# Kernel tuning notes

Measured on AMD Instinct MI355X. Metric: run time of the kernel, lower is better.

Reference implementation:

```python
import jax, jax.numpy as jnp
import numpy as np

B = 4096
IN_DIMS = (3, 32, 32)      # in_numel = 3072
OUT_DIMS = (64, 16, 16)    # out_numel = 16384
IN_NUMEL = int(np.prod(IN_DIMS))
OUT_NUMEL = int(np.prod(OUT_DIMS))


def setup_inputs() -> dict:
    key = jax.random.key(0)
    k1, k2, k3, k4 = jax.random.split(key, 4)
    x = jax.random.normal(k1, (B,) + IN_DIMS, dtype=jnp.float32)
    # Cached composed linear operator (out_numel x in_numel); scale ~1/sqrt(fan_in)
    cached_matrix = jax.random.normal(k2, (OUT_NUMEL, IN_NUMEL), dtype=jnp.float32) / np.sqrt(IN_NUMEL)
    cached_matrix_extra = jax.random.uniform(k3, (1,), dtype=jnp.float32) + 0.5
    cached_tensor_extra = jax.random.normal(k4, (IN_NUMEL, IN_NUMEL), dtype=jnp.float32) / IN_NUMEL
    return {
        "x": x,
        "cached_matrix": cached_matrix,
        "cached_matrix_extra": cached_matrix_extra,
        "cached_tensor_extra": cached_tensor_extra,
    }


def reference(x, cached_matrix, cached_matrix_extra, cached_tensor_extra):
    batches = x.shape[0]
    # input_as_matrix: [in_numel, B]
    X = x.reshape(batches, -1).T
    # input_as_matrix_extra: L2 norm per column -> [1, B]
    X_extra = jnp.linalg.norm(X, ord=2, axis=0, keepdims=True)
    # output_as_matrix = M @ X : [out_numel, B]
    Y = jnp.matmul(cached_matrix, X)
    # output_as_matrix_extra = s * ||x|| + sum((T @ X) * X, axis=0)
    Y_extra = cached_matrix_extra * X_extra + jnp.sum(jnp.matmul(cached_tensor_extra, X) * X, axis=0, keepdims=True)
    Y = Y / Y_extra
    return Y.T.reshape(batches, *OUT_DIMS)
```

## Files before the change

kernel.cpp:

```cpp
#include <hip/hip_runtime.h>
#include <hip/hip_bf16.h>

typedef __attribute__((ext_vector_type(8))) short bf16x8;
typedef __attribute__((ext_vector_type(4))) short bf16x4;
typedef __attribute__((ext_vector_type(4))) float f32x4;

#define DEV __device__ __forceinline__

static constexpr int BATCH = 4096;
static constexpr int KDIM  = 3072;
static constexpr int NOUT  = 16384;

DEV unsigned short f2bf(float f) {
  union { float f; unsigned int u; } v; v.f = f;
  unsigned int u = v.u;
  u += 0x7fffu + ((u >> 16) & 1u);
  return (unsigned short)(u >> 16);
}

DEV float bf2f(unsigned short h) {
  union { unsigned int u; float f; } v;
  v.u = ((unsigned int)h) << 16;
  return v.f;
}

__global__ __launch_bounds__(256) void prep_x_kernel(
    const float* __restrict__ x, unsigned short* __restrict__ xbf,
    float* __restrict__ nrm) {
  const int b = blockIdx.x;
  const int t = threadIdx.x;
  const float* row = x + (size_t)b * KDIM;
  unsigned short* orow = xbf + (size_t)b * KDIM;
  float ss = 0.f;
#pragma unroll
  for (int i = 0; i < 3; ++i) {
    const int c = i * 256 + t;
    float4 v = reinterpret_cast<const float4*>(row)[c];
    ss += v.x * v.x + v.y * v.y + v.z * v.z + v.w * v.w;
    bf16x4 o;
    o[0] = (short)f2bf(v.x); o[1] = (short)f2bf(v.y);
    o[2] = (short)f2bf(v.z); o[3] = (short)f2bf(v.w);
    reinterpret_cast<bf16x4*>(orow)[c] = o;
  }
#pragma unroll
  for (int off = 32; off > 0; off >>= 1) ss += __shfl_down(ss, off, 64);
  __shared__ float red[4];
  if ((t & 63) == 0) red[t >> 6] = ss;
  __syncthreads();
  if (t == 0) nrm[b] = sqrtf(red[0] + red[1] + red[2] + red[3]);
}

__global__ __launch_bounds__(256) void cvt_kernel(
    const float* __restrict__ src, unsigned short* __restrict__ dst, size_t n4) {
  size_t i = (size_t)blockIdx.x * blockDim.x + threadIdx.x;
  const size_t stride = (size_t)gridDim.x * blockDim.x;
  for (; i < n4; i += stride) {
    float4 v = reinterpret_cast<const float4*>(src)[i];
    bf16x4 o;
    o[0] = (short)f2bf(v.x); o[1] = (short)f2bf(v.y);
    o[2] = (short)f2bf(v.z); o[3] = (short)f2bf(v.w);
    reinterpret_cast<bf16x4*>(dst)[i] = o;
  }
}

__global__ __launch_bounds__(256) void finalize_ye_kernel(
    const float* __restrict__ nrm, const float* __restrict__ partial,
    const float* __restrict__ sp, float* __restrict__ ye) {
  const int b = blockIdx.x * blockDim.x + threadIdx.x;
  if (b >= BATCH) return;
  float qv = 0.f;
#pragma unroll
  for (int i = 0; i < 48; ++i) qv += partial[(size_t)b * 48 + i];
  ye[b] = sp[0] * nrm[b] + qv;
}

static constexpr int BK8 = 64;

#define LDSE(BUF, OP, HALF) ((BUF)*32768 + (OP)*16384 + (HALF)*8192)

#define STAGE8(OP, HALF, S, BUF)                                             \
  {                                                                          \
    const unsigned short* gb_ = (OP) ? Bm : A;                               \
    const int gr0_ = ((OP) ? col0 : row0) + (HALF)*128;                      \
    _Pragma("unroll")                                                        \
    for (int j_ = 0; j_ < 2; ++j_) {                                         \
      const int row_ = j_*64 + wid*8 + (lane >> 3);                          \
      const int le_  = ((lane & 7)*8) ^ ((row_ & 7) << 3);                   \
      __builtin_amdgcn_global_load_lds(                                      \
        (const __attribute__((address_space(1))) unsigned int*)(const void*) \
          (gb_ + (size_t)(gr0_ + row_)*KDIM + (S)*BK8 + le_),                \
        (__attribute__((address_space(3))) unsigned int*)(void*)             \
          (lds + LDSE(BUF, OP, HALF) + j_*4096 + wid*512),                   \
        16, 0, 0);                                                           \
    }                                                                        \
  }

#define LOADA8(P, QM, DST)                                                   \
  _Pragma("unroll")                                                          \
  for (int mi = 0; mi < 4; ++mi) {                                           \
    const int r_ = wm*64 + mi*16 + (lane & 15);                              \
    const int xv_ = (r_ & 7) << 3;                                           \
    _Pragma("unroll")                                                        \
    for (int ks = 0; ks < 2; ++ks)                                           \
      DST[mi][ks] = *reinterpret_cast<const bf16x8*>(                        \
          lds + LDSE(P, 0, QM) + ((r_*64 + ks*32 + (lane >> 4)*8) ^ xv_));   \
  }

#define LOADB8(P, QN, DST)                                                   \
  _Pragma("unroll")                                                          \
  for (int ni = 0; ni < 2; ++ni) {                                           \
    const int r_ = wn*32 + ni*16 + (lane & 15);                              \
    const int xv_ = (r_ & 7) << 3;                                           \
    _Pragma("unroll")                                                        \
    for (int ks = 0; ks < 2; ++ks)                                           \
      DST[ni][ks] = *reinterpret_cast<const bf16x8*>(                        \
          lds + LDSE(P, 1, QN) + ((r_*64 + ks*32 + (lane >> 4)*8) ^ xv_));   \
  }

#define MMA8(QM, QN, ASRC, BSRC)                                             \
  __builtin_amdgcn_s_setprio(1);                                             \
  _Pragma("unroll")                                                          \
  for (int mi = 0; mi < 4; ++mi)                                             \
    _Pragma("unroll")                                                        \
    for (int ni = 0; ni < 2; ++ni)                                           \
      _Pragma("unroll")                                                      \
      for (int ks = 0; ks < 2; ++ks)                                         \
        acc[(QM)*4 + mi][(QN)*2 + ni] =                                      \
            __builtin_amdgcn_mfma_f32_16x16x32_bf16(                         \
                ASRC[mi][ks], BSRC[ni][ks], acc[(QM)*4 + mi][(QN)*2 + ni],   \
                0, 0, 0);                                                    \
  __builtin_amdgcn_s_setprio(0);

#define VMW(N)                                                               \
  asm volatile("s_waitcnt vmcnt(" #N ")" ::: "memory");                      \
  __builtin_amdgcn_sched_barrier(0)

#define BARR __builtin_amdgcn_s_barrier()

#define TILE9(P, T)                                                          \
  LOADA8(P, 0, aft); LOADB8(P, 0, bft0);                                     \
  STAGE8(1, 1, (T)+1, (P)^1);                                                \
  BARR;                                                                      \
  STAGE8(1, 0, (T)+1, (P)^1);                                                \
  MMA8(0, 0, aft, bft0);                                                     \
  LOADB8(P, 1, bft1);                                                        \
  BARR;                                                                      \
  STAGE8(0, 0, (T)+2, P);                                                    \
  MMA8(0, 1, aft, bft1);                                                     \
  LOADA8(P, 1, aft);                                                         \
  BARR;                                                                      \
  MMA8(1, 1, aft, bft1);                                                     \
  BARR;                                                                      \
  STAGE8(0, 1, (T)+2, P);                                                    \
  MMA8(1, 0, aft, bft0);                                                     \
  VMW(4);                                                                    \
  BARR;

#define LGKMW8 asm volatile("s_waitcnt lgkmcnt(8)" ::: "memory")

#define TILE8Q(P, T)                                                         \
  LOADA8(P, 0, aft); LOADB8(P, 0, bft0);                                     \
  STAGE8(1, 1, (T)+1, (P)^1);                                                \
  LGKMW8;                                                                    \
  BARR; MMA8(0, 0, aft, bft0); BARR;                                         \
  LOADB8(P, 1, bft1);                                                        \
  STAGE8(1, 0, (T)+1, (P)^1);                                                \
  BARR; MMA8(0, 1, aft, bft1); BARR;                                         \
  LOADA8(P, 1, aft);                                                         \
  STAGE8(0, 0, (T)+2, P);                                                    \
  BARR; MMA8(1, 1, aft, bft1); BARR;                                         \
  STAGE8(0, 1, (T)+2, P);                                                    \
  BARR; MMA8(1, 0, aft, bft0); VMW(4); BARR;

#define PROLOG8Q(T0)                                                         \
  STAGE8(0, 0, (T0), 0); STAGE8(1, 0, (T0), 0);                              \
  STAGE8(0, 1, (T0), 0); STAGE8(1, 1, (T0), 0);                              \
  STAGE8(0, 0, (T0)+1, 1); STAGE8(0, 1, (T0)+1, 1);                          \
  VMW(4);                                                                    \
  BARR;

#define TAIL8Q(TE)                                                           \
  LOADA8(0, 0, aft); LOADB8(0, 0, bft0);                                     \
  STAGE8(1, 1, (TE)+1, 1);                                                   \
  BARR; MMA8(0, 0, aft, bft0); BARR;                                         \
  LOADB8(0, 1, bft1);                                                        \
  STAGE8(1, 0, (TE)+1, 1);                                                   \
  BARR; MMA8(0, 1, aft, bft1); BARR;                                         \
  LOADA8(0, 1, aft);                                                         \
  BARR; MMA8(1, 1, aft, bft1); BARR;                                         \
  MMA8(1, 0, aft, bft0); VMW(0); BARR;                                       \
  LOADA8(1, 0, aft); LOADB8(1, 0, bft0);                                     \
  BARR; MMA8(0, 0, aft, bft0); BARR;                                         \
  LOADB8(1, 1, bft1);                                                        \
  BARR; MMA8(0, 1, aft, bft1); BARR;                                         \
  LOADA8(1, 1, aft);                                                         \
  BARR; MMA8(1, 1, aft, bft1); BARR;                                         \
  MMA8(1, 0, aft, bft0);

__global__ __launch_bounds__(512) void gemm8_kernel(
    const unsigned short* __restrict__ A,
    const unsigned short* __restrict__ Bm,
    const float* __restrict__ ye,
    float* __restrict__ out) {
  __shared__ unsigned short lds[65536];
  const int t = threadIdx.x;
  const int lane = t & 63, wid = t >> 6;
  const int wm = wid >> 2, wn = wid & 3;

  const int bid = blockIdx.x;
  const int xcd = bid & 7, r = bid >> 3;
  const int by = r >> 3;
  const int bx = xcd * 8 + (r & 7);
  const int row0 = by * 256, col0 = bx * 256;

  f32x4 acc[8][4];
#pragma unroll
  for (int i = 0; i < 8; ++i)
#pragma unroll
    for (int j = 0; j < 4; ++j) acc[i][j] = (f32x4){0.f, 0.f, 0.f, 0.f};

  bf16x8 aft[4][2], bft0[2][2], bft1[2][2];

  STAGE8(1, 1, 0, 0); STAGE8(1, 0, 0, 0);
  STAGE8(0, 0, 0, 0); STAGE8(0, 1, 0, 0);
  STAGE8(0, 0, 1, 1); STAGE8(0, 1, 1, 1);
  VMW(4);
  BARR;

#pragma unroll 1
  for (int i = 0; i < 23; ++i) {
    const int t0 = 2 * i;
    TILE9(0, t0);
    TILE9(1, t0 + 1);
  }

  LOADA8(0, 0, aft); LOADB8(0, 0, bft0);
  STAGE8(1, 1, 47, 1);
  BARR;
  STAGE8(1, 0, 47, 1);
  MMA8(0, 0, aft, bft0);
  LOADB8(0, 1, bft1);
  BARR;
  MMA8(0, 1, aft, bft1);
  LOADA8(0, 1, aft);
  BARR;
  MMA8(1, 1, aft, bft1);
  BARR;
  MMA8(1, 0, aft, bft0);
  VMW(0);
  BARR;
  LOADA8(1, 0, aft); LOADB8(1, 0, bft0);
  BARR;
  MMA8(0, 0, aft, bft0);
  LOADB8(1, 1, bft1);
  BARR;
  MMA8(0, 1, aft, bft1);
  LOADA8(1, 1, aft);
  BARR;
  MMA8(1, 1, aft, bft1);
  BARR;
  MMA8(1, 0, aft, bft0);

#pragma unroll
  for (int am = 0; am < 8; ++am) {
#pragma unroll
    for (int j = 0; j < 4; ++j) {
      const int b = row0 + (am >> 2) * 128 + wm * 64 + (am & 3) * 16 +
                    (lane >> 4) * 4 + j;
      const float rr = 1.0f / ye[b];
      float* orow = out + (size_t)b * NOUT + col0;
#pragma unroll
      for (int an = 0; an < 4; ++an)
        orow[(an >> 1) * 128 + wn * 32 + (an & 1) * 16 + (lane & 15)] =
            acc[am][an][j] * rr;
    }
  }
}

__global__ __launch_bounds__(512) void qform8_kernel(
    const unsigned short* __restrict__ A,
    const unsigned short* __restrict__ Bm,
    float* __restrict__ partial) {
  __shared__ unsigned short lds[65536];
  const int t = threadIdx.x;
  const int lane = t & 63, wid = t >> 6;
  const int wm = wid >> 2, wn = wid & 3;

  const int bid = blockIdx.x;
  const int wgid = (bid & 7) * 96 + (bid >> 3);
  const int jt = wgid / 64;
  const int rem = wgid % 64;
  const int bt = rem >> 2;
  const int ks4 = rem & 3;
  const int row0 = bt * 256, col0 = jt * 256;
  const int k0t = ks4 * 12;

  f32x4 acc[8][4];
#pragma unroll
  for (int i = 0; i < 8; ++i)
#pragma unroll
    for (int j = 0; j < 4; ++j) acc[i][j] = (f32x4){0.f, 0.f, 0.f, 0.f};

  bf16x8 aft[4][2], bft0[2][2], bft1[2][2];

  PROLOG8Q(k0t);
#pragma unroll 1
  for (int i = 0; i < 5; ++i) {
    const int t0 = k0t + 2 * i;
    TILE8Q(0, t0);
    TILE8Q(1, t0 + 1);
  }
  TAIL8Q(k0t + 10);

  float* sred = reinterpret_cast<float*>(lds);
#pragma unroll
  for (int am = 0; am < 8; ++am) {
#pragma unroll
    for (int j = 0; j < 4; ++j) {
      const int b = row0 + (am >> 2) * 128 + wm * 64 + (am & 3) * 16 +
                    (lane >> 4) * 4 + j;
      float s = 0.f;
#pragma unroll
      for (int an = 0; an < 4; ++an) {
        const int col = col0 + (an >> 1) * 128 + wn * 32 + (an & 1) * 16 +
                        (lane & 15);
        s += acc[am][an][j] * bf2f(A[(size_t)b * KDIM + col]);
      }
      s += __shfl_xor(s, 1, 64);
      s += __shfl_xor(s, 2, 64);
      s += __shfl_xor(s, 4, 64);
      s += __shfl_xor(s, 8, 64);
      if ((lane & 15) == 0)
        sred[wid * 128 + am * 16 + j * 4 + (lane >> 4)] = s;
    }
  }
  __syncthreads();
  if (t < 256) {
    const int wmI = t >> 7, idx = t & 127;
    const int am = idx >> 4, j = (idx >> 2) & 3, lp = idx & 3;
    const int b = row0 + (am >> 2) * 128 + wmI * 64 + (am & 3) * 16 + lp * 4 + j;
    float s = 0.f;
#pragma unroll
    for (int w2 = 0; w2 < 4; ++w2) s += sred[(wmI * 4 + w2) * 128 + idx];
    partial[(size_t)b * 48 + jt * 4 + ks4] = s;
  }
}

__global__ __launch_bounds__(256) void main_gemm_kernel(
    const unsigned short* __restrict__ A,
    const float* __restrict__ Bf,
    const float* __restrict__ ye,
    float* __restrict__ out) {
  __shared__ unsigned short ldsA[128 * 32];
  __shared__ unsigned short ldsB[128 * 32];
  const int t = threadIdx.x;
  const int lane = t & 63;
  const int wv = t >> 6;
  const int wr = wv >> 1, wc = wv & 1;
  const int col0 = blockIdx.x * 128;
  const int row0 = blockIdx.y * 128;

  f32x4 acc[4][4];
#pragma unroll
  for (int i = 0; i < 4; ++i)
#pragma unroll
    for (int j = 0; j < 4; ++j) acc[i][j] = (f32x4){0.f, 0.f, 0.f, 0.f};

  const unsigned short* aBase = A + (size_t)row0 * KDIM;
  const float* bfBase = Bf + (size_t)col0 * KDIM;
  const int ldsoff0 = (t & ~63) * 8;

  for (int k0 = 0; k0 < KDIM; k0 += 32) {
    __syncthreads();
#pragma unroll
    for (int i = 0; i < 2; ++i) {
      const int c = i * 256 + t;
      const unsigned short* ga = aBase + (size_t)(c >> 2) * KDIM + (k0 + (c & 3) * 8);
      __builtin_amdgcn_global_load_lds(
          (const __attribute__((address_space(1))) unsigned int*)(const void*)ga,
          (__attribute__((address_space(3))) unsigned int*)(void*)(ldsA + i * 2048 + ldsoff0),
          16, 0, 0);
    }
#pragma unroll
    for (int i = 0; i < 2; ++i) {
      const int c = i * 256 + t;
      const int r = c >> 1, ko = (c & 1) * 16;
      const float* gp = bfBase + (size_t)r * KDIM + k0 + ko;
      unsigned short tmp[16];
#pragma unroll
      for (int q = 0; q < 4; ++q) {
        float4 v = reinterpret_cast<const float4*>(gp)[q];
        tmp[q * 4 + 0] = f2bf(v.x); tmp[q * 4 + 1] = f2bf(v.y);
        tmp[q * 4 + 2] = f2bf(v.z); tmp[q * 4 + 3] = f2bf(v.w);
      }
#pragma unroll
      for (int q = 0; q < 2; ++q)
        *reinterpret_cast<bf16x8*>(&ldsB[r * 32 + ko + q * 8]) =
            *reinterpret_cast<const bf16x8*>(&tmp[q * 8]);
    }
    __syncthreads();
    bf16x8 af[4], bfr[4];
#pragma unroll
    for (int mi = 0; mi < 4; ++mi)
      af[mi] = *reinterpret_cast<const bf16x8*>(
          &ldsA[(wr * 64 + mi * 16 + (lane & 15)) * 32 + (lane >> 4) * 8]);
#pragma unroll
    for (int ni = 0; ni < 4; ++ni)
      bfr[ni] = *reinterpret_cast<const bf16x8*>(
          &ldsB[(wc * 64 + ni * 16 + (lane & 15)) * 32 + (lane >> 4) * 8]);
#pragma unroll
    for (int mi = 0; mi < 4; ++mi)
#pragma unroll
      for (int ni = 0; ni < 4; ++ni)
        acc[mi][ni] = __builtin_amdgcn_mfma_f32_16x16x32_bf16(af[mi], bfr[ni], acc[mi][ni], 0, 0, 0);
  }

#pragma unroll
  for (int mi = 0; mi < 4; ++mi) {
#pragma unroll
    for (int j = 0; j < 4; ++j) {
      const int b = row0 + wr * 64 + mi * 16 + (lane >> 4) * 4 + j;
      const float rr = 1.0f / ye[b];
      float* orow = out + (size_t)b * NOUT + col0 + wc * 64 + (lane & 15);
#pragma unroll
      for (int ni = 0; ni < 4; ++ni) orow[ni * 16] = acc[mi][ni][j] * rr;
    }
  }
}

extern "C" void kernel_launch(void* const* d_in, const int* in_sizes, int n_in,
                              void* d_out, int out_size, void* d_ws, size_t ws_size,
                              hipStream_t stream) {
  (void)in_sizes; (void)n_in; (void)out_size;
  const float* x  = (const float*)d_in[0];
  const float* M  = (const float*)d_in[1];
  const float* sc = (const float*)d_in[2];
  const float* T  = (const float*)d_in[3];
  float* out = (float*)d_out;
  char* ws = (char*)d_ws;

  size_t off = 0;
  auto wsalloc = [&](size_t bytes) -> void* {
    void* p = ws + off;
    off += (bytes + 255) & ~(size_t)255;
    return p;
  };
  unsigned short* Xbf = (unsigned short*)wsalloc((size_t)BATCH * KDIM * 2);
  unsigned short* Tbf = (unsigned short*)wsalloc((size_t)KDIM * KDIM * 2);
  float* nrm = (float*)wsalloc((size_t)BATCH * 4);
  float* ye  = (float*)wsalloc((size_t)BATCH * 4);
  float* partial = (float*)wsalloc((size_t)BATCH * 48 * 4);
  unsigned short* Mbf = (unsigned short*)wsalloc((size_t)NOUT * KDIM * 2);
  const bool useMbf = (off <= ws_size);

  prep_x_kernel<<<BATCH, 256, 0, stream>>>(x, Xbf, nrm);
  cvt_kernel<<<1024, 256, 0, stream>>>(T, Tbf, (size_t)KDIM * KDIM / 4);
  if (useMbf)
    cvt_kernel<<<2048, 256, 0, stream>>>(M, Mbf, (size_t)NOUT * KDIM / 4);
  qform8_kernel<<<768, 512, 0, stream>>>(Xbf, Tbf, partial);
  finalize_ye_kernel<<<BATCH / 256, 256, 0, stream>>>(nrm, partial, sc, ye);
  if (useMbf)
    gemm8_kernel<<<1024, 512, 0, stream>>>(Xbf, Mbf, ye, out);
  else
    main_gemm_kernel<<<dim3(NOUT / 128, BATCH / 128), 256, 0, stream>>>(
        Xbf, M, ye, out);
}
```

Measured before the change: 551.3 us.

## Fuse T conversion into prep kernel and overlap M conversion with qform GEMM

Merges the x-prep and T-to-bf16 conversion into one launch by giving extra blocks the conversion job. The separate M-to-bf16 conversion kernel is removed, and its work is spread across the qform GEMM blocks, interleaved with the MMA tiles through software-pipelined float4 loads and stores. The goal is to hide the memory-bound conversion of M behind compute-bound quadratic-form work and to save launches. The cost is higher register pressure and more global traffic inside the qform kernel, which could slow its main loop.

After: 558.2 us. Within noise of the previous version (+1.2%).

```diff
diff --git a/kernel.cpp b/kernel.cpp
--- a/kernel.cpp
+++ b/kernel.cpp
@@ -24,42 +24,44 @@
   return v.f;
 }
 
-__global__ __launch_bounds__(256) void prep_x_kernel(
+DEV bf16x4 pk4(float4 v) {
+  bf16x4 o;
+  o[0] = (short)f2bf(v.x); o[1] = (short)f2bf(v.y);
+  o[2] = (short)f2bf(v.z); o[3] = (short)f2bf(v.w);
+  return o;
+}
+
+__global__ __launch_bounds__(256) void prep_cvtT_kernel(
     const float* __restrict__ x, unsigned short* __restrict__ xbf,
-    float* __restrict__ nrm) {
-  const int b = blockIdx.x;
+    float* __restrict__ nrm,
+    const float* __restrict__ T, unsigned short* __restrict__ tbf) {
+  __shared__ float red[4];
+  const int bid = blockIdx.x;
   const int t = threadIdx.x;
-  const float* row = x + (size_t)b * KDIM;
-  unsigned short* orow = xbf + (size_t)b * KDIM;
-  float ss = 0.f;
-#pragma unroll
-  for (int i = 0; i < 3; ++i) {
-    const int c = i * 256 + t;
-    float4 v = reinterpret_cast<const float4*>(row)[c];
-    ss += v.x * v.x + v.y * v.y + v.z * v.z + v.w * v.w;
-    bf16x4 o;
-    o[0] = (short)f2bf(v.x); o[1] = (short)f2bf(v.y);
-    o[2] = (short)f2bf(v.z); o[3] = (short)f2bf(v.w);
-    reinterpret_cast<bf16x4*>(orow)[c] = o;
-  }
-#pragma unroll
-  for (int off = 32; off > 0; off >>= 1) ss += __shfl_down(ss, off, 64);
-  __shared__ float red[4];
-  if ((t & 63) == 0) red[t >> 6] = ss;
-  __syncthreads();
-  if (t == 0) nrm[b] = sqrtf(red[0] + red[1] + red[2] + red[3]);
-}
-
-__global__ __launch_bounds__(256) void cvt_kernel(
-    const float* __restrict__ src, unsigned short* __restrict__ dst, size_t n4) {
-  size_t i = (size_t)blockIdx.x * blockDim.x + threadIdx.x;
-  const size_t stride = (size_t)gridDim.x * blockDim.x;
-  for (; i < n4; i += stride) {
-    float4 v = reinterpret_cast<const float4*>(src)[i];
-    bf16x4 o;
-    o[0] = (short)f2bf(v.x); o[1] = (short)f2bf(v.y);
-    o[2] = (short)f2bf(v.z); o[3] = (short)f2bf(v.w);
-    reinterpret_cast<bf16x4*>(dst)[i] = o;
+  if (bid < BATCH) {
+    const float* row = x + (size_t)bid * KDIM;
+    unsigned short* orow = xbf + (size_t)bid * KDIM;
+    float ss = 0.f;
+#pragma unroll
+    for (int i = 0; i < 3; ++i) {
+      const int c = i * 256 + t;
+      float4 v = reinterpret_cast<const float4*>(row)[c];
+      ss += v.x * v.x + v.y * v.y + v.z * v.z + v.w * v.w;
+      reinterpret_cast<bf16x4*>(orow)[c] = pk4(v);
+    }
+#pragma unroll
+    for (int off = 32; off > 0; off >>= 1) ss += __shfl_down(ss, off, 64);
+    if ((t & 63) == 0) red[t >> 6] = ss;
+    __syncthreads();
+    if (t == 0) nrm[bid] = sqrtf(red[0] + red[1] + red[2] + red[3]);
+  } else {
+    const int cb = bid - BATCH;
+    const size_t n4 = (size_t)KDIM * KDIM / 4;
+    const size_t stride = 1024 * 256;
+    for (size_t i = (size_t)cb * 256 + t; i < n4; i += stride) {
+      float4 v = reinterpret_cast<const float4*>(T)[i];
+      reinterpret_cast<bf16x4*>(tbf)[i] = pk4(v);
+    }
   }
 }
 
@@ -277,10 +279,32 @@
   }
 }
 
+#define CVT_EVEN(PT)                                                         \
+  if (DOCVT) {                                                               \
+    cb0 = Mf4[cvb + (size_t)(((PT)+1)*3    )*512];                           \
+    cb1 = Mf4[cvb + (size_t)(((PT)+1)*3 + 1)*512];                           \
+    cb2 = Mf4[cvb + (size_t)(((PT)+1)*3 + 2)*512];                           \
+    Mb4[cvb + (size_t)((PT)*3    )*512] = pk4(ca0);                          \
+    Mb4[cvb + (size_t)((PT)*3 + 1)*512] = pk4(ca1);                          \
+    Mb4[cvb + (size_t)((PT)*3 + 2)*512] = pk4(ca2);                          \
+  }
+#define CVT_ODD(PT)                                                          \
+  if (DOCVT) {                                                               \
+    ca0 = Mf4[cvb + (size_t)(((PT)+1)*3    )*512];                           \
+    ca1 = Mf4[cvb + (size_t)(((PT)+1)*3 + 1)*512];                           \
+    if ((PT) != 9) ca2 = Mf4[cvb + (size_t)(((PT)+1)*3 + 2)*512];            \
+    Mb4[cvb + (size_t)((PT)*3    )*512] = pk4(cb0);                          \
+    Mb4[cvb + (size_t)((PT)*3 + 1)*512] = pk4(cb1);                          \
+    Mb4[cvb + (size_t)((PT)*3 + 2)*512] = pk4(cb2);                          \
+  }
+
+template <int DOCVT>
 __global__ __launch_bounds__(512) void qform8_kernel(
     const unsigned short* __restrict__ A,
     const unsigned short* __restrict__ Bm,
-    float* __restrict__ partial) {
+    float* __restrict__ partial,
+    const float* __restrict__ Mf,
+    unsigned short* __restrict__ Mbf) {
   __shared__ unsigned short lds[65536];
   const int t = threadIdx.x;
   const int lane = t & 63, wid = t >> 6;
@@ -303,12 +327,28 @@
 
   bf16x8 aft[4][2], bft0[2][2], bft1[2][2];
 
+  const float4* Mf4 = reinterpret_cast<const float4*>(Mf);
+  bf16x4* Mb4 = reinterpret_cast<bf16x4*>(Mbf);
+  const size_t cvb = (size_t)bid * 16384 + t;
+  float4 ca0, ca1, ca2, cb0, cb1, cb2;
+  if (DOCVT) {
+    ca0 = Mf4[cvb];
+    ca1 = Mf4[cvb + 512];
+    ca2 = Mf4[cvb + 1024];
+  }
+
   PROLOG8Q(k0t);
 #pragma unroll 1
   for (int i = 0; i < 5; ++i) {
     const int t0 = k0t + 2 * i;
+    CVT_EVEN(2 * i);
     TILE8Q(0, t0);
+    CVT_ODD(2 * i + 1);
     TILE8Q(1, t0 + 1);
+  }
+  if (DOCVT) {
+    Mb4[cvb + (size_t)(30) * 512] = pk4(ca0);
+    Mb4[cvb + (size_t)(31) * 512] = pk4(ca1);
   }
   TAIL8Q(k0t + 10);
 
@@ -453,11 +493,11 @@
   unsigned short* Mbf = (unsigned short*)wsalloc((size_t)NOUT * KDIM * 2);
   const bool useMbf = (off <= ws_size);
 
-  prep_x_kernel<<<BATCH, 256, 0, stream>>>(x, Xbf, nrm);
-  cvt_kernel<<<1024, 256, 0, stream>>>(T, Tbf, (size_t)KDIM * KDIM / 4);
+  prep_cvtT_kernel<<<BATCH + 1024, 256, 0, stream>>>(x, Xbf, nrm, T, Tbf);
   if (useMbf)
-    cvt_kernel<<<2048, 256, 0, stream>>>(M, Mbf, (size_t)NOUT * KDIM / 4);
-  qform8_kernel<<<768, 512, 0, stream>>>(Xbf, Tbf, partial);
+    qform8_kernel<1><<<768, 512, 0, stream>>>(Xbf, Tbf, partial, M, Mbf);
+  else
+    qform8_kernel<0><<<768, 512, 0, stream>>>(Xbf, Tbf, partial, M, Mbf);
   finalize_ye_kernel<<<BATCH / 256, 256, 0, stream>>>(nrm, partial, sc, ye);
   if (useMbf)
     gemm8_kernel<<<1024, 512, 0, stream>>>(Xbf, Mbf, ye, out);
```
